# Optimization experiments

Measured on AMD Instinct MI355X. Metric: run time of the kernel, lower is better.

Reference implementation:

```python
import jax, jax.numpy as jnp
import numpy as np

N_NODES = 50000
N_EDGES = 800000
F = 64
EPS = 1e-5


def batchnorm(x, gamma, beta):
    # training-mode BatchNorm1d: batch mean, biased variance
    mu = jnp.mean(x, axis=0)
    var = jnp.mean((x - mu) ** 2, axis=0)
    return gamma * (x - mu) * jax.lax.rsqrt(var + EPS) + beta


def setup_inputs() -> dict:
    key = jax.random.key(0)
    ks = jax.random.split(key, 10)
    s = 1.0 / np.sqrt(3 * F)
    return {
        "node_feats": jax.random.normal(ks[0], (N_NODES, F), jnp.float32),
        "edge_feats": jax.random.normal(ks[1], (N_EDGES, F), jnp.float32),
        "src": jax.random.randint(ks[2], (N_EDGES,), 0, N_NODES, jnp.int32),
        "dst": jax.random.randint(ks[3], (N_EDGES,), 0, N_NODES, jnp.int32),
        "W_mlpt": jax.random.uniform(ks[4], (3 * F, F), jnp.float32, -s, s),
        "b_mlpt": jnp.zeros((F,), jnp.float32),
        "g_mlpt": jnp.ones((F,), jnp.float32),
        "be_mlpt": jnp.zeros((F,), jnp.float32),
        "W_gate": jax.random.uniform(ks[5], (3 * F, F), jnp.float32, -s, s),
        "b_gate": jnp.zeros((F,), jnp.float32),
        "g_gate": jnp.ones((F,), jnp.float32),
        "be_gate": jnp.zeros((F,), jnp.float32),
        "g_node": jnp.ones((F,), jnp.float32),
        "be_node": jnp.zeros((F,), jnp.float32),
    }


def reference(node_feats, edge_feats, src, dst,
              W_mlpt, b_mlpt, g_mlpt, be_mlpt,
              W_gate, b_gate, g_gate, be_gate,
              g_node, be_node):
    # edge-wise gather + concat: [E, 3F]
    h_cat = jnp.concatenate(
        [node_feats[src], node_feats[dst], edge_feats], axis=1)
    # two small MLPs: Linear + BN + activation (dropout p=0)
    h_mlpt = jax.nn.sigmoid(batchnorm(h_cat @ W_mlpt + b_mlpt, g_mlpt, be_mlpt))
    h_gate = jax.nn.softplus(batchnorm(h_cat @ W_gate + b_gate, g_gate, be_gate))
    h_upd = h_mlpt * h_gate  # [E, F]
    # scatter-sum messages onto destination nodes
    agg = jax.ops.segment_sum(h_upd, dst, num_segments=N_NODES)  # [N, F]
    node_out = jax.nn.sigmoid(batchnorm(agg, g_node, be_node) + node_feats)
    return (node_out, edge_feats)
```

## Files before the change

### kernel.cpp

```cpp
#include <hip/hip_runtime.h>

#define E_TOT   800000
#define NN      50000
#define FF      64

typedef __attribute__((ext_vector_type(8))) short  short8;
typedef __attribute__((ext_vector_type(4))) float  f32x4;

__device__ __forceinline__ unsigned short f2bf(float f) {
  union { float f; unsigned int u; } v; v.f = f;
  unsigned int r = v.u + 0x7fffu + ((v.u >> 16) & 1u);
  return (unsigned short)(r >> 16);
}

__device__ __forceinline__ unsigned int pkbf(float a, float b) {
  unsigned int r;
  asm("v_cvt_pk_bf16_f32 %0, %1, %2" : "=v"(r) : "v"(a), "v"(b));
  return r;
}

__device__ __forceinline__ void atomic_pk_bf16(unsigned short* p, unsigned int v) {
  asm volatile("global_atomic_pk_add_bf16 %0, %1, off" :: "v"(p), "v"(v) : "memory");
}

__device__ __forceinline__ float bflo(unsigned int u) { return __uint_as_float(u << 16); }
__device__ __forceinline__ float bfhi(unsigned int u) { return __uint_as_float(u & 0xffff0000u); }

__device__ __forceinline__ float sigmoidf_(float x) {
  return 1.f / (1.f + __expf(-x));
}

__global__ void pack_w(const float* __restrict__ Wm, const float* __restrict__ Wg,
                       unsigned short* __restrict__ Wp) {
  int t = blockIdx.x * 256 + threadIdx.x;
  if (t >= 3072) return;
  int lane = t & 63;
  int kk   = (t >> 6) % 6;
  int mnt  = t / 384;
  const float* W = (mnt >> 2) ? Wg : Wm;
  int nt  = mnt & 3;
  int col = nt * 16 + (lane & 15);
  int kb  = kk * 32 + (lane >> 4) * 8;
  #pragma unroll
  for (int j = 0; j < 8; ++j)
    Wp[t * 8 + j] = f2bf(W[(kb + j) * 64 + col]);
}

__global__ __launch_bounds__(256, 5)
void edge_gemm(const float* __restrict__ nodef, const float* __restrict__ edgef,
               const int* __restrict__ src, const int* __restrict__ dst,
               const unsigned short* __restrict__ Wp,
               float* __restrict__ stats,
               uint4* __restrict__ Yw,
               float* __restrict__ outE, int write_copy)
{
  __shared__ unsigned short sh[64 * 200];
  __shared__ float red[4 * 256];

  const int tid = threadIdx.x;
  const int e0  = blockIdx.x * 64;
  const int row = tid >> 2;
  const int cq  = tid & 3;

  const int s = src[e0 + row], d = dst[e0 + row];
  const float* ps = nodef + (size_t)s * 64 + cq * 4;
  const float* pd = nodef + (size_t)d * 64 + cq * 4;
  const float* pe = edgef + (size_t)(e0 + row) * 64 + cq * 4;
  unsigned short* sp = &sh[row * 200 + cq * 4];

  float4 ev[4];
  #pragma unroll
  for (int it = 0; it < 4; ++it) {
    float4 v0 = *(const float4*)(ps + it * 16);
    float4 v1 = *(const float4*)(pd + it * 16);
    float4 v2 = *(const float4*)(pe + it * 16);
    ev[it] = v2;
    *(uint2*)(sp +   0 + it * 16) = make_uint2(pkbf(v0.x, v0.y), pkbf(v0.z, v0.w));
    *(uint2*)(sp +  64 + it * 16) = make_uint2(pkbf(v1.x, v1.y), pkbf(v1.z, v1.w));
    *(uint2*)(sp + 128 + it * 16) = make_uint2(pkbf(v2.x, v2.y), pkbf(v2.z, v2.w));
  }
  if (write_copy) {
    float4* op = (float4*)(outE + (size_t)(e0 + row) * 64 + cq * 4);
    #pragma unroll
    for (int it = 0; it < 4; ++it) op[it * 4] = ev[it];
  }
  __syncthreads();

  const int w = tid >> 6, lane = tid & 63;
  f32x4 acc[8] = {};
  const unsigned short* abase = &sh[(w * 16 + (lane & 15)) * 200 + (lane >> 4) * 8];
  const short8* wp = (const short8*)Wp;

  #pragma unroll
  for (int kk = 0; kk < 6; ++kk) {
    short8 a = *(const short8*)(abase + kk * 32);
    #pragma unroll
    for (int nt = 0; nt < 8; ++nt) {
      short8 b = wp[(nt * 6 + kk) * 64 + lane];
      acc[nt] = __builtin_amdgcn_mfma_f32_16x16x32_bf16(a, b, acc[nt], 0, 0, 0);
    }
  }

  uint4* yb = Yw + (((size_t)blockIdx.x * 4 + w) * 4) * 64 + lane;
  #pragma unroll
  for (int ntp = 0; ntp < 4; ++ntp) {
    uint4 q;
    q.x = pkbf(acc[2 * ntp][0],     acc[2 * ntp][1]);
    q.y = pkbf(acc[2 * ntp][2],     acc[2 * ntp][3]);
    q.z = pkbf(acc[2 * ntp + 1][0], acc[2 * ntp + 1][1]);
    q.w = pkbf(acc[2 * ntp + 1][2], acc[2 * ntp + 1][3]);
    yb[ntp * 64] = q;
  }

  #pragma unroll
  for (int nt = 0; nt < 8; ++nt) {
    float sv = acc[nt][0] + acc[nt][1] + acc[nt][2] + acc[nt][3];
    float qv = acc[nt][0] * acc[nt][0] + acc[nt][1] * acc[nt][1] +
               acc[nt][2] * acc[nt][2] + acc[nt][3] * acc[nt][3];
    sv += __shfl_xor(sv, 16); sv += __shfl_xor(sv, 32);
    qv += __shfl_xor(qv, 16); qv += __shfl_xor(qv, 32);
    if ((lane >> 4) == 0) {
      red[w * 256 + nt * 16 + lane]       = sv;
      red[w * 256 + 128 + nt * 16 + lane] = qv;
    }
  }
  __syncthreads();
  float v = red[tid] + red[256 + tid] + red[512 + tid] + red[768 + tid];
  atomicAdd(&stats[(blockIdx.x & 63) * 256 + tid], v);
}

__global__ void finalize_edge(const float* __restrict__ stats,
                              const float* __restrict__ g_m, const float* __restrict__ be_m,
                              const float* __restrict__ g_g, const float* __restrict__ be_g,
                              float* __restrict__ coef) {
  int c = threadIdx.x;
  float s = 0.f, q = 0.f;
  for (int sl = 0; sl < 64; ++sl) { s += stats[sl * 256 + c]; q += stats[sl * 256 + 128 + c]; }
  float mu  = s * (1.f / E_TOT);
  float var = fmaxf(q * (1.f / E_TOT) - mu * mu, 0.f);
  float g   = (c < 64) ? g_m[c]  : g_g[c - 64];
  float be  = (c < 64) ? be_m[c] : be_g[c - 64];
  float a   = g * rsqrtf(var + 1e-5f);
  coef[c]       = a;
  coef[128 + c] = be - mu * a;
}

__global__ __launch_bounds__(256)
void edge_apply(const uint4* __restrict__ Yw, const int* __restrict__ dst,
                const float* __restrict__ coef,
                unsigned short* __restrict__ aggb)
{
  const int tid = threadIdx.x;
  const int w = tid >> 6, lane = tid & 63;
  const int e0 = blockIdx.x * 64;
  const int r0 = w * 16 + ((lane >> 4) << 2);
  const int4 dn = *(const int4*)&dst[e0 + r0];
  const int colb = lane & 15;
  const int par  = colb & 1;

  const uint4* yb = Yw + (((size_t)blockIdx.x * 4 + w) * 4) * 64 + lane;
  uint4 qm0 = yb[0], qm1 = yb[64], qg0 = yb[128], qg1 = yb[192];
  const unsigned int um[8] = {qm0.x, qm0.y, qm0.z, qm0.w, qm1.x, qm1.y, qm1.z, qm1.w};
  const unsigned int ug[8] = {qg0.x, qg0.y, qg0.z, qg0.w, qg1.x, qg1.y, qg1.z, qg1.w};
  const int dr[4] = {dn.x, dn.y, dn.z, dn.w};

  #pragma unroll
  for (int ntm = 0; ntm < 4; ++ntm) {
    const int col = ntm * 16 + colb;
    const float am = coef[col],      cm = coef[128 + col];
    const float ag = coef[64 + col], cg = coef[192 + col];
    float hv[4];
    #pragma unroll
    for (int p = 0; p < 2; ++p) {
      unsigned int m = um[ntm * 2 + p], g = ug[ntm * 2 + p];
      #pragma unroll
      for (int h = 0; h < 2; ++h) {
        float mv = h ? bfhi(m) : bflo(m);
        float gv = h ? bfhi(g) : bflo(g);
        float ym = fmaf(mv, am, cm);
        float yg = fmaf(gv, ag, cg);
        float sig = sigmoidf_(ym);
        float sp  = (yg > 20.f) ? yg : __logf(1.f + __expf(yg));
        hv[2 * p + h] = sig * sp;
      }
    }
    float pv[4];
    #pragma unroll
    for (int r = 0; r < 4; ++r) pv[r] = __shfl_xor(hv[r], 1);
    const int colp = ntm * 16 + (colb & ~1);
    #pragma unroll
    for (int rr = 0; rr < 2; ++rr) {
      int r = par * 2 + rr;
      float lo = par ? pv[r] : hv[r];
      float hi = par ? hv[r] : pv[r];
      atomic_pk_bf16(&aggb[(size_t)dr[r] * 64 + colp], pkbf(lo, hi));
    }
  }
}

__global__ void node_stats(const unsigned int* __restrict__ aggu, float* __restrict__ nstats) {
  __shared__ float rs0[256], rq0[256], rs1[256], rq1[256];
  int tid = threadIdx.x;
  int cp = tid & 31;
  float s0 = 0.f, q0 = 0.f, s1 = 0.f, q1 = 0.f;
  for (int r = blockIdx.x * 8 + (tid >> 5); r < NN; r += gridDim.x * 8) {
    unsigned int u = aggu[r * 32 + cp];
    float v0 = bflo(u), v1 = bfhi(u);
    s0 += v0; q0 += v0 * v0; s1 += v1; q1 += v1 * v1;
  }
  rs0[tid] = s0; rq0[tid] = q0; rs1[tid] = s1; rq1[tid] = q1;
  __syncthreads();
  if (tid < 32) {
    s0 = 0.f; q0 = 0.f; s1 = 0.f; q1 = 0.f;
    #pragma unroll
    for (int k = 0; k < 8; ++k) {
      s0 += rs0[tid + 32 * k]; q0 += rq0[tid + 32 * k];
      s1 += rs1[tid + 32 * k]; q1 += rq1[tid + 32 * k];
    }
    int slot = blockIdx.x & 31;
    atomicAdd(&nstats[slot * 128 + 2 * tid],      s0);
    atomicAdd(&nstats[slot * 128 + 2 * tid + 1],  s1);
    atomicAdd(&nstats[slot * 128 + 64 + 2 * tid],     q0);
    atomicAdd(&nstats[slot * 128 + 64 + 2 * tid + 1], q1);
  }
}

__global__ void finalize_node(const float* __restrict__ nstats,
                              const float* __restrict__ g_n, const float* __restrict__ be_n,
                              float* __restrict__ coefn) {
  int c = threadIdx.x;
  float s = 0.f, q = 0.f;
  for (int sl = 0; sl < 32; ++sl) { s += nstats[sl * 128 + c]; q += nstats[sl * 128 + 64 + c]; }
  float mu  = s * (1.f / NN);
  float var = fmaxf(q * (1.f / NN) - mu * mu, 0.f);
  float a   = g_n[c] * rsqrtf(var + 1e-5f);
  coefn[c]      = a;
  coefn[64 + c] = be_n[c] - mu * a;
}

__global__ void node_out_k(float* __restrict__ out, const unsigned int* __restrict__ aggu,
                           const float* __restrict__ nodef, const float* __restrict__ coefn) {
  int i  = blockIdx.x * 256 + threadIdx.x;
  int cb = (i & 15) * 4;
  uint2  u  = ((const uint2*)aggu)[i];
  float4 nf = ((const float4*)nodef)[i];
  float4 r;
  r.x = sigmoidf_(coefn[cb + 0] * bflo(u.x) + coefn[64 + cb + 0] + nf.x);
  r.y = sigmoidf_(coefn[cb + 1] * bfhi(u.x) + coefn[64 + cb + 1] + nf.y);
  r.z = sigmoidf_(coefn[cb + 2] * bflo(u.y) + coefn[64 + cb + 2] + nf.z);
  r.w = sigmoidf_(coefn[cb + 3] * bfhi(u.y) + coefn[64 + cb + 3] + nf.w);
  ((float4*)out)[i] = r;
}

extern "C" void kernel_launch(void* const* d_in, const int* in_sizes, int n_in,
                              void* d_out, int out_size, void* d_ws, size_t ws_size,
                              hipStream_t stream) {
  const float* nodef = (const float*)d_in[0];
  const float* edgef = (const float*)d_in[1];
  const int*   src   = (const int*)d_in[2];
  const int*   dst   = (const int*)d_in[3];
  const float* W_m   = (const float*)d_in[4];
  const float* g_m   = (const float*)d_in[6];
  const float* be_m  = (const float*)d_in[7];
  const float* W_g   = (const float*)d_in[8];
  const float* g_g   = (const float*)d_in[10];
  const float* be_g  = (const float*)d_in[11];
  const float* g_n   = (const float*)d_in[12];
  const float* be_n  = (const float*)d_in[13];

  float* out  = (float*)d_out;
  float* outE = out + (size_t)NN * FF;

  char* ws = (char*)d_ws;
  unsigned short* aggb = (unsigned short*)ws;
  float* stats  = (float*)(ws + 0x640000);
  float* coef   = (float*)(ws + 0x650000);
  float* nstats = (float*)(ws + 0x651000);
  float* coefn  = (float*)(ws + 0x655000);
  unsigned short* Wp = (unsigned short*)(ws + 0x656000);

  const size_t y_bytes = (size_t)E_TOT * 128 * 2;
  const int y_in_ws = (ws_size >= (size_t)0x700000 + y_bytes);
  uint4* Yw = y_in_ws ? (uint4*)(ws + 0x700000) : (uint4*)outE;

  hipMemsetAsync(aggb, 0, (size_t)NN * FF * 2, stream);
  hipMemsetAsync(stats, 0, 0x15200, stream);

  pack_w<<<12, 256, 0, stream>>>(W_m, W_g, Wp);
  edge_gemm<<<E_TOT / 64, 256, 0, stream>>>(nodef, edgef, src, dst, Wp,
                                            stats, Yw, outE, y_in_ws);
  finalize_edge<<<1, 128, 0, stream>>>(stats, g_m, be_m, g_g, be_g, coef);
  edge_apply<<<E_TOT / 64, 256, 0, stream>>>(Yw, dst, coef, aggb);
  if (!y_in_ws) {
    hipMemcpyAsync(outE, edgef, (size_t)E_TOT * FF * sizeof(float),
                   hipMemcpyDeviceToDevice, stream);
  }
  node_stats<<<512, 256, 0, stream>>>((const unsigned int*)aggb, nstats);
  finalize_node<<<1, 64, 0, stream>>>(nstats, g_n, be_n, coefn);
  node_out_k<<<NN * FF / 4 / 256, 256, 0, stream>>>(out, (const unsigned int*)aggb,
                                                    nodef, coefn);
}
```

Baseline: 431.4 us.

## Sort edges by destination and replace per-edge atomics with segmented reduction

```diff
diff --git a/kernel.cpp b/kernel.cpp
--- a/kernel.cpp
+++ b/kernel.cpp
@@ -46,12 +46,57 @@
     Wp[t * 8 + j] = f2bf(W[(kb + j) * 64 + col]);
 }
 
+__global__ void hist_k(const int* __restrict__ dst, int* __restrict__ counts) {
+  int e = blockIdx.x * 256 + threadIdx.x;
+  if (e < E_TOT) atomicAdd(&counts[dst[e]], 1);
+}
+
+__global__ __launch_bounds__(1024)
+void scan_k(const int* __restrict__ counts, int* __restrict__ cursor) {
+  __shared__ int wsum[16];
+  const int t = threadIdx.x;
+  const int CH = 49;
+  int lo = t * CH, hi = min(lo + CH, NN);
+  if (lo > NN) lo = NN;
+  int s = 0;
+  for (int i = lo; i < hi; ++i) s += counts[i];
+  int lane = t & 63, w = t >> 6;
+  int v = s;
+  #pragma unroll
+  for (int dlt = 1; dlt < 64; dlt <<= 1) {
+    int u = __shfl_up(v, dlt);
+    if (lane >= dlt) v += u;
+  }
+  if (lane == 63) wsum[w] = v;
+  __syncthreads();
+  if (t == 0) {
+    int a = 0;
+    for (int i = 0; i < 16; ++i) { int c = wsum[i]; wsum[i] = a; a += c; }
+  }
+  __syncthreads();
+  int run = v - s + wsum[w];
+  for (int i = lo; i < hi; ++i) {
+    int c = counts[i];
+    cursor[i] = run;
+    run += c;
+  }
+}
+
+__global__ void fill_k(const int* __restrict__ dst, int* __restrict__ cursor,
+                       int* __restrict__ eid) {
+  int e = blockIdx.x * 256 + threadIdx.x;
+  if (e < E_TOT) {
+    int p = atomicAdd(&cursor[dst[e]], 1);
+    eid[p] = e;
+  }
+}
+
 __global__ __launch_bounds__(256, 5)
 void edge_gemm(const float* __restrict__ nodef, const float* __restrict__ edgef,
                const int* __restrict__ src, const int* __restrict__ dst,
                const unsigned short* __restrict__ Wp,
                float* __restrict__ stats,
-               uint4* __restrict__ Yw,
+               unsigned int* __restrict__ Y,
                float* __restrict__ outE, int write_copy)
 {
   __shared__ unsigned short sh[64 * 200];
@@ -84,7 +129,8 @@
     #pragma unroll
     for (int it = 0; it < 4; ++it) op[it * 4] = ev[it];
   }
-  __syncthreads();
+
+  asm volatile("s_waitcnt lgkmcnt(0)" ::: "memory");
 
   const int w = tid >> 6, lane = tid & 63;
   f32x4 acc[8] = {};
@@ -101,15 +147,21 @@
     }
   }
 
-  uint4* yb = Yw + (((size_t)blockIdx.x * 4 + w) * 4) * 64 + lane;
-  #pragma unroll
-  for (int ntp = 0; ntp < 4; ++ntp) {
-    uint4 q;
-    q.x = pkbf(acc[2 * ntp][0],     acc[2 * ntp][1]);
-    q.y = pkbf(acc[2 * ntp][2],     acc[2 * ntp][3]);
-    q.z = pkbf(acc[2 * ntp + 1][0], acc[2 * ntp + 1][1]);
-    q.w = pkbf(acc[2 * ntp + 1][2], acc[2 * ntp + 1][3]);
-    yb[ntp * 64] = q;
+  asm volatile("s_waitcnt lgkmcnt(0)" ::: "memory");
+
+  unsigned int* shu = (unsigned int*)sh;
+  const int colb = lane & 15, rq = lane >> 4, par = colb & 1;
+  #pragma unroll
+  for (int nt = 0; nt < 8; ++nt) {
+    float hv0 = acc[nt][0], hv1 = acc[nt][1], hv2 = acc[nt][2], hv3 = acc[nt][3];
+    float pv0 = __shfl_xor(hv0, 1), pv1 = __shfl_xor(hv1, 1);
+    float pv2 = __shfl_xor(hv2, 1), pv3 = __shfl_xor(hv3, 1);
+    float loA = par ? pv2 : hv0,  hiA = par ? hv2 : pv0;
+    float loB = par ? pv3 : hv1,  hiB = par ? hv3 : pv1;
+    int r0 = rq * 4 + par * 2;
+    int ci = nt * 8 + (colb >> 1);
+    shu[(w * 16 + r0)     * 100 + ci] = pkbf(loA, hiA);
+    shu[(w * 16 + r0 + 1) * 100 + ci] = pkbf(loB, hiB);
   }
 
   #pragma unroll
@@ -125,6 +177,15 @@
     }
   }
   __syncthreads();
+
+  #pragma unroll
+  for (int k2 = 0; k2 < 4; ++k2) {
+    int k  = tid + k2 * 256;
+    int rw = k >> 4, part = k & 15;
+    uint4 v = *(const uint4*)&shu[rw * 100 + part * 4];
+    *(uint4*)&Y[(size_t)(e0 + rw) * 64 + part * 4] = v;
+  }
+
   float v = red[tid] + red[256 + tid] + red[512 + tid] + red[768 + tid];
   atomicAdd(&stats[(blockIdx.x & 63) * 256 + tid], v);
 }
@@ -146,56 +207,54 @@
 }
 
 __global__ __launch_bounds__(256)
-void edge_apply(const uint4* __restrict__ Yw, const int* __restrict__ dst,
-                const float* __restrict__ coef,
-                unsigned short* __restrict__ aggb)
+void node_sum(const unsigned int* __restrict__ Yu, const int* __restrict__ eid,
+              const int* __restrict__ dst, const float* __restrict__ coef,
+              unsigned short* __restrict__ aggb)
 {
-  const int tid = threadIdx.x;
-  const int w = tid >> 6, lane = tid & 63;
-  const int e0 = blockIdx.x * 64;
-  const int r0 = w * 16 + ((lane >> 4) << 2);
-  const int4 dn = *(const int4*)&dst[e0 + r0];
-  const int colb = lane & 15;
-  const int par  = colb & 1;
-
-  const uint4* yb = Yw + (((size_t)blockIdx.x * 4 + w) * 4) * 64 + lane;
-  uint4 qm0 = yb[0], qm1 = yb[64], qg0 = yb[128], qg1 = yb[192];
-  const unsigned int um[8] = {qm0.x, qm0.y, qm0.z, qm0.w, qm1.x, qm1.y, qm1.z, qm1.w};
-  const unsigned int ug[8] = {qg0.x, qg0.y, qg0.z, qg0.w, qg1.x, qg1.y, qg1.z, qg1.w};
-  const int dr[4] = {dn.x, dn.y, dn.z, dn.w};
-
-  #pragma unroll
-  for (int ntm = 0; ntm < 4; ++ntm) {
-    const int col = ntm * 16 + colb;
-    const float am = coef[col],      cm = coef[128 + col];
-    const float ag = coef[64 + col], cg = coef[192 + col];
-    float hv[4];
-    #pragma unroll
-    for (int p = 0; p < 2; ++p) {
-      unsigned int m = um[ntm * 2 + p], g = ug[ntm * 2 + p];
-      #pragma unroll
-      for (int h = 0; h < 2; ++h) {
-        float mv = h ? bfhi(m) : bflo(m);
-        float gv = h ? bfhi(g) : bflo(g);
-        float ym = fmaf(mv, am, cm);
-        float yg = fmaf(gv, ag, cg);
-        float sig = sigmoidf_(ym);
-        float sp  = (yg > 20.f) ? yg : __logf(1.f + __expf(yg));
-        hv[2 * p + h] = sig * sp;
-      }
-    }
-    float pv[4];
-    #pragma unroll
-    for (int r = 0; r < 4; ++r) pv[r] = __shfl_xor(hv[r], 1);
-    const int colp = ntm * 16 + (colb & ~1);
-    #pragma unroll
-    for (int rr = 0; rr < 2; ++rr) {
-      int r = par * 2 + rr;
-      float lo = par ? pv[r] : hv[r];
-      float hi = par ? hv[r] : pv[r];
-      atomic_pk_bf16(&aggb[(size_t)dr[r] * 64 + colp], pkbf(lo, hi));
-    }
-  }
+  const int tid  = threadIdx.x;
+  const int w    = tid >> 6, lane = tid & 63;
+  const int base = (blockIdx.x * 4 + w) * 64;
+  const int l    = lane & 31;
+  const bool hi  = lane >= 32;
+
+  const float A0 = hi ? coef[64 + 2 * l]  : coef[2 * l];
+  const float A1 = hi ? coef[65 + 2 * l]  : coef[2 * l + 1];
+  const float C0 = hi ? coef[192 + 2 * l] : coef[128 + 2 * l];
+  const float C1 = hi ? coef[193 + 2 * l] : coef[128 + 2 * l + 1];
+
+  const int el = eid[base + lane];
+  const int dl = dst[el];
+
+  float a0 = 0.f, a1 = 0.f;
+  int dcur = __shfl(dl, 0);
+
+  auto flush = [&]() {
+    if (!hi) atomic_pk_bf16(&aggb[(size_t)dcur * 64 + 2 * l], pkbf(a0, a1));
+  };
+  auto accum = [&](unsigned int y) {
+    float f0 = bflo(y), f1 = bfhi(y);
+    float v0 = fmaf(f0, A0, C0), v1 = fmaf(f1, A1, C1);
+    float x0 = __expf(hi ? v0 : -v0), x1 = __expf(hi ? v1 : -v1);
+    float r0 = hi ? ((v0 > 20.f) ? v0 : __logf(1.f + x0)) : 1.f / (1.f + x0);
+    float r1 = hi ? ((v1 > 20.f) ? v1 : __logf(1.f + x1)) : 1.f / (1.f + x1);
+    float p0 = __shfl_xor(r0, 32), p1 = __shfl_xor(r1, 32);
+    a0 += r0 * p0; a1 += r1 * p1;
+  };
+
+  unsigned int yA = Yu[(size_t)__shfl(el, 0) * 64 + lane];
+  unsigned int yB = Yu[(size_t)__shfl(el, 1) * 64 + lane];
+
+  for (int j = 0; j < 64; j += 2) {
+    int dj0 = __shfl(dl, j);
+    if (dj0 != dcur) { flush(); dcur = dj0; a0 = a1 = 0.f; }
+    accum(yA);
+    if (j + 2 < 64) yA = Yu[(size_t)__shfl(el, j + 2) * 64 + lane];
+    int dj1 = __shfl(dl, j + 1);
+    if (dj1 != dcur) { flush(); dcur = dj1; a0 = a1 = 0.f; }
+    accum(yB);
+    if (j + 3 < 64) yB = Yu[(size_t)__shfl(el, j + 3) * 64 + lane];
+  }
+  flush();
 }
 
 __global__ void node_stats(const unsigned int* __restrict__ aggu, float* __restrict__ nstats) {
@@ -270,6 +329,7 @@
 
   float* out  = (float*)d_out;
   float* outE = out + (size_t)NN * FF;
+  int*   eid  = (int*)d_out;
 
   char* ws = (char*)d_ws;
   unsigned short* aggb = (unsigned short*)ws;
@@ -278,19 +338,25 @@
   float* nstats = (float*)(ws + 0x651000);
   float* coefn  = (float*)(ws + 0x655000);
   unsigned short* Wp = (unsigned short*)(ws + 0x656000);
-
-  const size_t y_bytes = (size_t)E_TOT * 128 * 2;
+  int* counts = (int*)(ws + 0x670000);
+  int* cursor = (int*)(ws + 0x6B0000);
+
+  const size_t y_bytes = (size_t)E_TOT * 64 * 4;
   const int y_in_ws = (ws_size >= (size_t)0x700000 + y_bytes);
-  uint4* Yw = y_in_ws ? (uint4*)(ws + 0x700000) : (uint4*)outE;
+  unsigned int* Y = y_in_ws ? (unsigned int*)(ws + 0x700000) : (unsigned int*)outE;
 
   hipMemsetAsync(aggb, 0, (size_t)NN * FF * 2, stream);
   hipMemsetAsync(stats, 0, 0x15200, stream);
-
+  hipMemsetAsync(counts, 0, NN * sizeof(int), stream);
+
+  hist_k<<<(E_TOT + 255) / 256, 256, 0, stream>>>(dst, counts);
   pack_w<<<12, 256, 0, stream>>>(W_m, W_g, Wp);
   edge_gemm<<<E_TOT / 64, 256, 0, stream>>>(nodef, edgef, src, dst, Wp,
-                                            stats, Yw, outE, y_in_ws);
+                                            stats, Y, outE, y_in_ws);
+  scan_k<<<1, 1024, 0, stream>>>(counts, cursor);
   finalize_edge<<<1, 128, 0, stream>>>(stats, g_m, be_m, g_g, be_g, coef);
-  edge_apply<<<E_TOT / 64, 256, 0, stream>>>(Yw, dst, coef, aggb);
+  fill_k<<<(E_TOT + 255) / 256, 256, 0, stream>>>(dst, cursor, eid);
+  node_sum<<<E_TOT / 64 / 4, 256, 0, stream>>>(Y, eid, dst, coef, aggb);
   if (!y_in_ws) {
     hipMemcpyAsync(outE, edgef, (size_t)E_TOT * FF * sizeof(float),
                    hipMemcpyDeviceToDevice, stream);
```

Result: slower. 524.0 us (+21.5%).
